# Optimization experiments

Measured on AMD Instinct MI355X. Metric: run time of the kernel, lower is better.

The kernel has to match this reference:

```python
import jax, jax.numpy as jnp
import numpy as np

B, S, DIN, DQ, DK = 8, 2048, 1024, 64, 64

def setup_inputs() -> dict:
    key = jax.random.key(0)
    ks = jax.random.split(key, 8)
    sc = 0.02
    return {
        "input_tensor": jax.random.normal(ks[0], (B, S, DIN), jnp.float32),
        "attention_mask": jax.random.randint(ks[1], (B, 1, S), 0, 2) == 1,
        "Wq": jax.random.normal(ks[2], (DIN, DQ), jnp.float32) * sc,
        "bq": jnp.zeros((DQ,), jnp.float32),
        "Wk": jax.random.normal(ks[3], (DIN, DK), jnp.float32) * sc,
        "bk": jnp.zeros((DK,), jnp.float32),
        "Wv": jax.random.normal(ks[4], (DIN, DK), jnp.float32) * sc,
        "bv": jnp.zeros((DK,), jnp.float32),
    }

def reference(input_tensor, attention_mask, Wq, bq, Wk, bk, Wv, bv):
    q = input_tensor @ Wq + bq          # [B,S,DQ]
    k = input_tensor @ Wk + bk          # [B,S,DK]
    v = input_tensor @ Wv + bv          # [B,S,DK]
    # NOTE: original scales by sqrt(query.size(1)) == sqrt(seq_len), faithfully kept
    scale = q.shape[1] ** 0.5
    scores = jnp.einsum('bqd,bkd->bqk', q, k) / scale
    scores = jnp.where(attention_mask, jnp.float32(-1e9), scores)
    attn = jax.nn.softmax(scores, axis=-1)
    context = jnp.einsum('bqk,bkd->bqd', attn, v)
    return context
```

## Files before the change

### kernel.cpp

```cpp
#include <hip/hip_runtime.h>
#include <hip/hip_bf16.h>

#define NB 8
#define SEQ 2048
#define DIN 1024
#define DH 64

typedef __attribute__((ext_vector_type(8))) short bf16x8;
typedef __attribute__((ext_vector_type(4))) float f32x4;

static __device__ __forceinline__ unsigned short f2bf(float f) {
    unsigned int u = __builtin_bit_cast(unsigned int, f);
    unsigned int r = (u + 0x7FFFu + ((u >> 16) & 1u)) >> 16;
    return (unsigned short)r;
}

static __device__ __forceinline__ unsigned int cvt_pk_bf16(float lo, float hi) {
    unsigned int d;
    asm volatile("v_cvt_pk_bf16_f32 %0, %1, %2" : "=v"(d) : "v"(lo), "v"(hi));
    return d;
}

__global__ __launch_bounds__(256) void prep_kernel(
    const float* __restrict__ Wq, const float* __restrict__ Wk, const float* __restrict__ Wv,
    unsigned short* __restrict__ Wfrag)
{
    int j = blockIdx.x * 256 + threadIdx.x;
    int mat = j >> 16;
    int rem = j & 65535;
    int k = rem >> 6;
    int c = rem & 63;
    const float* W = (mat == 0) ? Wq : ((mat == 1) ? Wk : Wv);
    float v = W[rem];
    int col = mat * 64 + c;
    int cg = col >> 4, cl = col & 15;
    int kk = k >> 5, kq = (k >> 3) & 3, ke = k & 7;
    Wfrag[(size_t)(cg * 32 + kk) * 512 + cl * 32 + kq * 8 + ke] = f2bf(v);
}

__global__ __launch_bounds__(256, 4) void qkv_kernel(
    const float* __restrict__ X, const unsigned short* __restrict__ Wfrag,
    const float* __restrict__ bq, const float* __restrict__ bk, const float* __restrict__ bv,
    unsigned short* __restrict__ Qb, unsigned short* __restrict__ Kb, unsigned short* __restrict__ Vt)
{
    __shared__ __align__(16) short As[16][128];

    const int tid = threadIdx.x;
    const int w   = tid >> 6;
    const int l15 = tid & 15;
    const int lq  = (tid & 63) >> 4;
    const int row0 = blockIdx.x * 16;

    f32x4 acc[3] = {};

    const int srow = tid >> 4;
    const int scol = (tid & 15) * 8;
    const float* xb = X + (size_t)(row0 + srow) * DIN + scol;
    const int swc = scol ^ ((srow & 7) << 3);

    const unsigned short* wfb[3];
    #pragma unroll
    for (int n = 0; n < 3; ++n)
        wfb[n] = Wfrag + (size_t)((w * 3 + n) * 32) * 512 + (l15 * 4 + lq) * 8;

    float4 pa0 = *(const float4*)(xb);
    float4 pa1 = *(const float4*)(xb + 4);
    float4 pb0 = *(const float4*)(xb + 128);
    float4 pb1 = *(const float4*)(xb + 132);

    #pragma unroll
    for (int step = 0; step < 8; ++step) {
        float4 c0 = (step & 1) ? pb0 : pa0;
        float4 c1 = (step & 1) ? pb1 : pa1;
        unsigned int u0 = cvt_pk_bf16(c0.x, c0.y);
        unsigned int u1 = cvt_pk_bf16(c0.z, c0.w);
        unsigned int u2 = cvt_pk_bf16(c1.x, c1.y);
        unsigned int u3 = cvt_pk_bf16(c1.z, c1.w);

        if (step + 2 < 8) {
            const float* xn = xb + (step + 2) * 128;
            if (step & 1) { pb0 = *(const float4*)(xn); pb1 = *(const float4*)(xn + 4); }
            else          { pa0 = *(const float4*)(xn); pa1 = *(const float4*)(xn + 4); }
        }

        __syncthreads();
        uint4 pk; pk.x = u0; pk.y = u1; pk.z = u2; pk.w = u3;
        *(uint4*)&As[srow][swc] = pk;
        __syncthreads();

        #pragma unroll
        for (int kkl = 0; kkl < 4; ++kkl) {
            bf16x8 bfr[3];
            #pragma unroll
            for (int n = 0; n < 3; ++n)
                bfr[n] = *(const bf16x8*)(wfb[n] + (size_t)(step * 4 + kkl) * 512);
            bf16x8 a = *(const bf16x8*)&As[l15][(kkl * 32 + lq * 8) ^ ((l15 & 7) << 3)];
            #pragma unroll
            for (int n = 0; n < 3; ++n)
                acc[n] = __builtin_amdgcn_mfma_f32_16x16x32_bf16(a, bfr[n], acc[n], 0, 0, 0);
        }
    }

    #pragma unroll
    for (int n = 0; n < 3; ++n) {
        int col = w * 48 + n * 16 + l15;
        int mat = col >> 6, c = col & 63;
        float badd = ((mat == 0) ? bq : ((mat == 1) ? bk : bv))[c];
        #pragma unroll
        for (int reg = 0; reg < 4; ++reg) {
            int row = row0 + lq * 4 + reg;
            unsigned short v16 = f2bf(acc[n][reg] + badd);
            if (mat == 0)      Qb[(size_t)row * DH + c] = v16;
            else if (mat == 1) Kb[(size_t)row * DH + c] = v16;
            else {
                int bb = row >> 11, ss = row & 2047;
                Vt[((size_t)(bb * DH + c)) * SEQ + ss] = v16;
            }
        }
    }
}

#define KT 128
#define NT (SEQ / KT)
#define PPITCH 36

__global__ __launch_bounds__(512, 2) void attn_kernel(
    const unsigned short* __restrict__ Qb, const unsigned short* __restrict__ Kb,
    const unsigned short* __restrict__ Vt, const int* __restrict__ mask,
    float* __restrict__ out)
{
    __shared__ __align__(16) unsigned char smem[65536 + 8 * 32 * PPITCH * 2 + 8 * 32 * 4];
    short (*Ks)[KT][DH]     = reinterpret_cast<short (*)[KT][DH]>(smem);
    short (*Vs)[DH][KT]     = reinterpret_cast<short (*)[DH][KT]>(smem + 32768);
    short (*ps)[32][PPITCH] = reinterpret_cast<short (*)[32][PPITCH]>(smem + 65536);
    float (*sml)[32]        = reinterpret_cast<float (*)[32]>(smem + 65536 + 8 * 32 * PPITCH * 2);
    float (*so)[64][64]     = reinterpret_cast<float (*)[64][64]>(smem);

    const int tid = threadIdx.x;
    const int w   = tid >> 6;
    const int l   = tid & 63;
    const int l15 = l & 15;
    const int lq  = l >> 4;
    const int wqh = w >> 2;
    const int wkq = w & 3;

    int bid = blockIdx.x;
    bid = (bid & 7) * 32 + (bid >> 3);
    const int b  = bid >> 5;
    const int q0 = (bid & 31) * 64;

    bf16x8 aq[2][2];
    #pragma unroll
    for (int m = 0; m < 2; ++m)
        #pragma unroll
        for (int kk = 0; kk < 2; ++kk)
            aq[m][kk] = *(const bf16x8*)(Qb + ((size_t)(b * SEQ + q0 + wqh * 32 + m * 16 + l15)) * DH + kk * 32 + lq * 8);

    const int krow = tid >> 3;
    const int kcol = (tid & 7) * 8;
    const int kdst = kcol ^ ((krow & 7) << 3);
    const int vrow = tid >> 4;
    const int vcol = (tid & 15) * 8;
    const int vdst = vcol ^ ((vrow & 7) << 3);

    const unsigned short* Kbase = Kb + (size_t)(b * SEQ) * DH + kcol;
    const unsigned short* Vbase = Vt + (size_t)(b * DH) * SEQ + vcol;

    bf16x8 kr[2], vr[2];
    #pragma unroll
    for (int i = 0; i < 2; ++i) {
        kr[i] = *(const bf16x8*)(Kbase + (size_t)(i * 64 + krow) * DH);
        vr[i] = *(const bf16x8*)(Vbase + (size_t)(i * 32 + vrow) * SEQ);
    }

    f32x4 o[2][4];
    #pragma unroll
    for (int m = 0; m < 2; ++m)
        #pragma unroll
        for (int n = 0; n < 4; ++n) o[m][n] = f32x4{0, 0, 0, 0};
    float lr[2][4] = {};

    const float rscale = 0.022097086912079612f;
    const int kw = wkq * 32;
    const int* mbase = mask + b * SEQ + kw + l15;

    for (int t = 0; t < NT; ++t) {
        const int cur = t & 1;

        #pragma unroll
        for (int i = 0; i < 2; ++i) *(bf16x8*)&Ks[cur][i * 64 + krow][kdst] = kr[i];
        #pragma unroll
        for (int i = 0; i < 2; ++i) *(bf16x8*)&Vs[cur][i * 32 + vrow][vdst] = vr[i];

        int mk0 = mbase[t * KT];
        int mk1 = mbase[t * KT + 16];

        if (t + 1 < NT) {
            const int key0n = (t + 1) * KT;
            #pragma unroll
            for (int i = 0; i < 2; ++i) {
                kr[i] = *(const bf16x8*)(Kbase + (size_t)(key0n + i * 64 + krow) * DH);
                vr[i] = *(const bf16x8*)(Vbase + (size_t)(i * 32 + vrow) * SEQ + key0n);
            }
        }

        __syncthreads();

        bf16x8 bkf[2][2];
        #pragma unroll
        for (int n = 0; n < 2; ++n)
            #pragma unroll
            for (int kk = 0; kk < 2; ++kk)
                bkf[n][kk] = *(const bf16x8*)&Ks[cur][kw + n * 16 + l15][(kk * 32 + lq * 8) ^ ((l15 & 7) << 3)];
        f32x4 s[2][2];
        #pragma unroll
        for (int m = 0; m < 2; ++m)
            #pragma unroll
            for (int n = 0; n < 2; ++n) s[m][n] = f32x4{0, 0, 0, 0};
        #pragma unroll
        for (int kk = 0; kk < 2; ++kk)
            #pragma unroll
            for (int m = 0; m < 2; ++m)
                #pragma unroll
                for (int n = 0; n < 2; ++n)
                    s[m][n] = __builtin_amdgcn_mfma_f32_16x16x32_bf16(aq[m][kk], bkf[n][kk], s[m][n], 0, 0, 0);

        float bb0 = mk0 ? -1e30f : 0.0f;
        float bb1 = mk1 ? -1e30f : 0.0f;
        #pragma unroll
        for (int m = 0; m < 2; ++m)
            #pragma unroll
            for (int n = 0; n < 2; ++n) {
                float bvv = n ? bb1 : bb0;
                #pragma unroll
                for (int r = 0; r < 4; ++r) {
                    float p = __expf(fmaf(s[m][n][r], rscale, bvv));
                    lr[m][r] += p;
                    ps[w][m * 16 + lq * 4 + r][n * 16 + l15] = (short)f2bf(p);
                }
            }

        bf16x8 pa[2];
        #pragma unroll
        for (int m = 0; m < 2; ++m)
            pa[m] = *(const bf16x8*)&ps[w][m * 16 + l15][lq * 8];
        bf16x8 bvf[4];
        #pragma unroll
        for (int n = 0; n < 4; ++n)
            bvf[n] = *(const bf16x8*)&Vs[cur][n * 16 + l15][(kw + lq * 8) ^ ((l15 & 7) << 3)];
        #pragma unroll
        for (int m = 0; m < 2; ++m)
            #pragma unroll
            for (int n = 0; n < 4; ++n)
                o[m][n] = __builtin_amdgcn_mfma_f32_16x16x32_bf16(pa[m], bvf[n], o[m][n], 0, 0, 0);
    }

    #pragma unroll
    for (int off = 1; off < 16; off <<= 1)
        #pragma unroll
        for (int m = 0; m < 2; ++m)
            #pragma unroll
            for (int r = 0; r < 4; ++r) lr[m][r] += __shfl_xor(lr[m][r], off);
    if (l15 == 0) {
        #pragma unroll
        for (int m = 0; m < 2; ++m)
            #pragma unroll
            for (int r = 0; r < 4; ++r) sml[w][m * 16 + lq * 4 + r] = lr[m][r];
    }
    __syncthreads();

    #pragma unroll
    for (int m = 0; m < 2; ++m)
        #pragma unroll
        for (int n = 0; n < 4; ++n)
            #pragma unroll
            for (int r = 0; r < 4; ++r)
                so[wkq][wqh * 32 + m * 16 + lq * 4 + r][n * 16 + l15] = o[m][n][r];
    __syncthreads();

    {
        int q  = tid >> 3;
        int d0 = (tid & 7) * 8;
        int wb = (q >> 5) * 4;
        float lt = sml[wb][q & 31] + sml[wb + 1][q & 31] + sml[wb + 2][q & 31] + sml[wb + 3][q & 31];
        float inv = 1.0f / lt;
        float vx[8];
        #pragma unroll
        for (int j = 0; j < 8; ++j)
            vx[j] = (so[0][q][d0 + j] + so[1][q][d0 + j] + so[2][q][d0 + j] + so[3][q][d0 + j]) * inv;
        float* op = out + ((size_t)(b * SEQ + q0 + q)) * DH + d0;
        float4 r0; r0.x = vx[0]; r0.y = vx[1]; r0.z = vx[2]; r0.w = vx[3];
        float4 r1; r1.x = vx[4]; r1.y = vx[5]; r1.z = vx[6]; r1.w = vx[7];
        *(float4*)op = r0;
        *(float4*)(op + 4) = r1;
    }
}

extern "C" void kernel_launch(void* const* d_in, const int* in_sizes, int n_in,
                              void* d_out, int out_size, void* d_ws, size_t ws_size,
                              hipStream_t stream) {
    const float* X    = (const float*)d_in[0];
    const int*   mask = (const int*)d_in[1];
    const float* Wq   = (const float*)d_in[2];
    const float* bq   = (const float*)d_in[3];
    const float* Wk   = (const float*)d_in[4];
    const float* bk   = (const float*)d_in[5];
    const float* Wv   = (const float*)d_in[6];
    const float* bv   = (const float*)d_in[7];
    float* out = (float*)d_out;

    char* ws = (char*)d_ws;
    unsigned short* Qb = (unsigned short*)(ws);
    unsigned short* Kb = (unsigned short*)(ws + (2u << 20));
    unsigned short* Vt = (unsigned short*)(ws + (4u << 20));
    unsigned short* Wfrag = (unsigned short*)(ws + (6u << 20));

    prep_kernel<<<768, 256, 0, stream>>>(Wq, Wk, Wv, Wfrag);
    qkv_kernel<<<1024, 256, 0, stream>>>(X, Wfrag, bq, bk, bv, Qb, Kb, Vt);
    attn_kernel<<<256, 512, 0, stream>>>(Qb, Kb, Vt, mask, out);
}
```

Measured before the change: 66.98 us.

## Enlarge QKV row tile with weight prefetch; single-buffer attention LDS for occupancy

The QKV projection now handles 32 rows per block instead of 16, with double-buffered LDS for the activation tile and a three-deep register prefetch of weight fragments, so each weight load feeds twice the MFMAs. The attention kernel drops from double-buffered K/V LDS to a single buffer with an extra barrier per tile, and merges partial outputs serially into one padded buffer. Together these halve attention LDS so more blocks can be resident. The cost is more barriers and a serialized reduction in attention, and fewer, heavier QKV blocks.

New measurement: 60.47 us. 9.7% less time.

```diff
diff --git a/kernel.cpp b/kernel.cpp
--- a/kernel.cpp
+++ b/kernel.cpp
@@ -38,66 +38,91 @@
     Wfrag[(size_t)(cg * 32 + kk) * 512 + cl * 32 + kq * 8 + ke] = f2bf(v);
 }
 
-__global__ __launch_bounds__(256, 4) void qkv_kernel(
+__global__ __launch_bounds__(256, 2) void qkv_kernel(
     const float* __restrict__ X, const unsigned short* __restrict__ Wfrag,
     const float* __restrict__ bq, const float* __restrict__ bk, const float* __restrict__ bv,
     unsigned short* __restrict__ Qb, unsigned short* __restrict__ Kb, unsigned short* __restrict__ Vt)
 {
-    __shared__ __align__(16) short As[16][128];
+    __shared__ __align__(16) short As[2][32][128];
 
     const int tid = threadIdx.x;
     const int w   = tid >> 6;
-    const int l15 = tid & 15;
-    const int lq  = (tid & 63) >> 4;
-    const int row0 = blockIdx.x * 16;
-
-    f32x4 acc[3] = {};
-
-    const int srow = tid >> 4;
-    const int scol = (tid & 15) * 8;
-    const float* xb = X + (size_t)(row0 + srow) * DIN + scol;
-    const int swc = scol ^ ((srow & 7) << 3);
+    const int l   = tid & 63;
+    const int l15 = l & 15;
+    const int lq  = l >> 4;
+    const int row0 = blockIdx.x * 32;
+
+    f32x4 acc[2][3] = {};
+
+    const float* xb = X + (size_t)row0 * DIN;
 
     const unsigned short* wfb[3];
     #pragma unroll
     for (int n = 0; n < 3; ++n)
         wfb[n] = Wfrag + (size_t)((w * 3 + n) * 32) * 512 + (l15 * 4 + lq) * 8;
 
-    float4 pa0 = *(const float4*)(xb);
-    float4 pa1 = *(const float4*)(xb + 4);
-    float4 pb0 = *(const float4*)(xb + 128);
-    float4 pb1 = *(const float4*)(xb + 132);
+    float4 pf[2][4];
+    #pragma unroll
+    for (int i = 0; i < 4; ++i) {
+        int c = tid + 256 * i;
+        const float* p = xb + (size_t)(c >> 5) * DIN + (c & 31) * 4;
+        pf[0][i] = *(const float4*)(p);
+        pf[1][i] = *(const float4*)(p + 128);
+    }
+
+    bf16x8 wb[3][3];
+    #pragma unroll
+    for (int n = 0; n < 3; ++n) wb[0][n] = *(const bf16x8*)(wfb[n]);
+    #pragma unroll
+    for (int n = 0; n < 3; ++n) wb[1][n] = *(const bf16x8*)(wfb[n] + 512);
 
     #pragma unroll
     for (int step = 0; step < 8; ++step) {
-        float4 c0 = (step & 1) ? pb0 : pa0;
-        float4 c1 = (step & 1) ? pb1 : pa1;
-        unsigned int u0 = cvt_pk_bf16(c0.x, c0.y);
-        unsigned int u1 = cvt_pk_bf16(c0.z, c0.w);
-        unsigned int u2 = cvt_pk_bf16(c1.x, c1.y);
-        unsigned int u3 = cvt_pk_bf16(c1.z, c1.w);
-
+        const int pi = step & 1;
+
+        unsigned int u[8];
+        #pragma unroll
+        for (int i = 0; i < 4; ++i) {
+            u[2 * i]     = cvt_pk_bf16(pf[pi][i].x, pf[pi][i].y);
+            u[2 * i + 1] = cvt_pk_bf16(pf[pi][i].z, pf[pi][i].w);
+        }
+        #pragma unroll
+        for (int i = 0; i < 4; ++i) {
+            int c = tid + 256 * i;
+            int r = c >> 5;
+            int bo = ((c & 31) * 8) ^ ((r & 7) << 4);
+            uint2 v2; v2.x = u[2 * i]; v2.y = u[2 * i + 1];
+            *(uint2*)((char*)&As[pi][r][0] + bo) = v2;
+        }
         if (step + 2 < 8) {
-            const float* xn = xb + (step + 2) * 128;
-            if (step & 1) { pb0 = *(const float4*)(xn); pb1 = *(const float4*)(xn + 4); }
-            else          { pa0 = *(const float4*)(xn); pa1 = *(const float4*)(xn + 4); }
-        }
-
+            #pragma unroll
+            for (int i = 0; i < 4; ++i) {
+                int c = tid + 256 * i;
+                pf[pi][i] = *(const float4*)(xb + (size_t)(c >> 5) * DIN + (step + 2) * 128 + (c & 31) * 4);
+            }
+        }
         __syncthreads();
-        uint4 pk; pk.x = u0; pk.y = u1; pk.z = u2; pk.w = u3;
-        *(uint4*)&As[srow][swc] = pk;
-        __syncthreads();
 
         #pragma unroll
         for (int kkl = 0; kkl < 4; ++kkl) {
-            bf16x8 bfr[3];
-            #pragma unroll
-            for (int n = 0; n < 3; ++n)
-                bfr[n] = *(const bf16x8*)(wfb[n] + (size_t)(step * 4 + kkl) * 512);
-            bf16x8 a = *(const bf16x8*)&As[l15][(kkl * 32 + lq * 8) ^ ((l15 & 7) << 3)];
-            #pragma unroll
-            for (int n = 0; n < 3; ++n)
-                acc[n] = __builtin_amdgcn_mfma_f32_16x16x32_bf16(a, bfr[n], acc[n], 0, 0, 0);
+            const int c = step * 4 + kkl;
+            if (c + 2 < 32) {
+                #pragma unroll
+                for (int n = 0; n < 3; ++n)
+                    wb[(c + 2) % 3][n] = *(const bf16x8*)(wfb[n] + (size_t)(c + 2) * 512);
+            }
+            bf16x8 a[2];
+            #pragma unroll
+            for (int m = 0; m < 2; ++m) {
+                int r = m * 16 + l15;
+                int bo = ((kkl * 32 + lq * 8) * 2) ^ ((r & 7) << 4);
+                a[m] = *(const bf16x8*)((const char*)&As[pi][r][0] + bo);
+            }
+            #pragma unroll
+            for (int m = 0; m < 2; ++m)
+                #pragma unroll
+                for (int n = 0; n < 3; ++n)
+                    acc[m][n] = __builtin_amdgcn_mfma_f32_16x16x32_bf16(a[m], wb[c % 3][n], acc[m][n], 0, 0, 0);
         }
     }
 
@@ -107,14 +132,17 @@
         int mat = col >> 6, c = col & 63;
         float badd = ((mat == 0) ? bq : ((mat == 1) ? bk : bv))[c];
         #pragma unroll
-        for (int reg = 0; reg < 4; ++reg) {
-            int row = row0 + lq * 4 + reg;
-            unsigned short v16 = f2bf(acc[n][reg] + badd);
-            if (mat == 0)      Qb[(size_t)row * DH + c] = v16;
-            else if (mat == 1) Kb[(size_t)row * DH + c] = v16;
-            else {
-                int bb = row >> 11, ss = row & 2047;
-                Vt[((size_t)(bb * DH + c)) * SEQ + ss] = v16;
+        for (int m = 0; m < 2; ++m) {
+            #pragma unroll
+            for (int reg = 0; reg < 4; ++reg) {
+                int row = row0 + m * 16 + lq * 4 + reg;
+                unsigned short v16 = f2bf(acc[m][n][reg] + badd);
+                if (mat == 0)      Qb[(size_t)row * DH + c] = v16;
+                else if (mat == 1) Kb[(size_t)row * DH + c] = v16;
+                else {
+                    int bb = row >> 11, ss = row & 2047;
+                    Vt[((size_t)(bb * DH + c)) * SEQ + ss] = v16;
+                }
             }
         }
     }
@@ -124,17 +152,17 @@
 #define NT (SEQ / KT)
 #define PPITCH 36
 
-__global__ __launch_bounds__(512, 2) void attn_kernel(
+__global__ __launch_bounds__(512, 4) void attn_kernel(
     const unsigned short* __restrict__ Qb, const unsigned short* __restrict__ Kb,
     const unsigned short* __restrict__ Vt, const int* __restrict__ mask,
     float* __restrict__ out)
 {
-    __shared__ __align__(16) unsigned char smem[65536 + 8 * 32 * PPITCH * 2 + 8 * 32 * 4];
-    short (*Ks)[KT][DH]     = reinterpret_cast<short (*)[KT][DH]>(smem);
-    short (*Vs)[DH][KT]     = reinterpret_cast<short (*)[DH][KT]>(smem + 32768);
-    short (*ps)[32][PPITCH] = reinterpret_cast<short (*)[32][PPITCH]>(smem + 65536);
-    float (*sml)[32]        = reinterpret_cast<float (*)[32]>(smem + 65536 + 8 * 32 * PPITCH * 2);
-    float (*so)[64][64]     = reinterpret_cast<float (*)[64][64]>(smem);
+    __shared__ __align__(16) unsigned char smem[32768 + 8 * 32 * PPITCH * 2 + 8 * 32 * 4];
+    short (*Ks)[DH]         = reinterpret_cast<short (*)[DH]>(smem);
+    short (*Vs)[KT]         = reinterpret_cast<short (*)[KT]>(smem + 16384);
+    short (*ps)[32][PPITCH] = reinterpret_cast<short (*)[32][PPITCH]>(smem + 32768);
+    float (*sml)[32]        = reinterpret_cast<float (*)[32]>(smem + 32768 + 8 * 32 * PPITCH * 2);
+    float (*Om)[68]         = reinterpret_cast<float (*)[68]>(smem);
 
     const int tid = threadIdx.x;
     const int w   = tid >> 6;
@@ -185,12 +213,10 @@
     const int* mbase = mask + b * SEQ + kw + l15;
 
     for (int t = 0; t < NT; ++t) {
-        const int cur = t & 1;
-
-        #pragma unroll
-        for (int i = 0; i < 2; ++i) *(bf16x8*)&Ks[cur][i * 64 + krow][kdst] = kr[i];
-        #pragma unroll
-        for (int i = 0; i < 2; ++i) *(bf16x8*)&Vs[cur][i * 32 + vrow][vdst] = vr[i];
+        #pragma unroll
+        for (int i = 0; i < 2; ++i) *(bf16x8*)&Ks[i * 64 + krow][kdst] = kr[i];
+        #pragma unroll
+        for (int i = 0; i < 2; ++i) *(bf16x8*)&Vs[i * 32 + vrow][vdst] = vr[i];
 
         int mk0 = mbase[t * KT];
         int mk1 = mbase[t * KT + 16];
@@ -211,7 +237,7 @@
         for (int n = 0; n < 2; ++n)
             #pragma unroll
             for (int kk = 0; kk < 2; ++kk)
-                bkf[n][kk] = *(const bf16x8*)&Ks[cur][kw + n * 16 + l15][(kk * 32 + lq * 8) ^ ((l15 & 7) << 3)];
+                bkf[n][kk] = *(const bf16x8*)&Ks[kw + n * 16 + l15][(kk * 32 + lq * 8) ^ ((l15 & 7) << 3)];
         f32x4 s[2][2];
         #pragma unroll
         for (int m = 0; m < 2; ++m)
@@ -247,12 +273,14 @@
         bf16x8 bvf[4];
         #pragma unroll
         for (int n = 0; n < 4; ++n)
-            bvf[n] = *(const bf16x8*)&Vs[cur][n * 16 + l15][(kw + lq * 8) ^ ((l15 & 7) << 3)];
+            bvf[n] = *(const bf16x8*)&Vs[n * 16 + l15][(kw + lq * 8) ^ ((l15 & 7) << 3)];
         #pragma unroll
         for (int m = 0; m < 2; ++m)
             #pragma unroll
             for (int n = 0; n < 4; ++n)
                 o[m][n] = __builtin_amdgcn_mfma_f32_16x16x32_bf16(pa[m], bvf[n], o[m][n], 0, 0, 0);
+
+        __syncthreads();
     }
 
     #pragma unroll
@@ -267,15 +295,24 @@
             #pragma unroll
             for (int r = 0; r < 4; ++r) sml[w][m * 16 + lq * 4 + r] = lr[m][r];
     }
-    __syncthreads();
-
-    #pragma unroll
-    for (int m = 0; m < 2; ++m)
-        #pragma unroll
-        for (int n = 0; n < 4; ++n)
-            #pragma unroll
-            for (int r = 0; r < 4; ++r)
-                so[wkq][wqh * 32 + m * 16 + lq * 4 + r][n * 16 + l15] = o[m][n][r];
+
+    #pragma unroll
+    for (int rnd = 0; rnd < 4; ++rnd) {
+        __syncthreads();
+        if (wkq == rnd) {
+            #pragma unroll
+            for (int m = 0; m < 2; ++m)
+                #pragma unroll
+                for (int n = 0; n < 4; ++n)
+                    #pragma unroll
+                    for (int r = 0; r < 4; ++r) {
+                        int row = wqh * 32 + m * 16 + lq * 4 + r;
+                        int col = n * 16 + l15;
+                        if (rnd == 0) Om[row][col] = o[m][n][r];
+                        else          Om[row][col] += o[m][n][r];
+                    }
+        }
+    }
     __syncthreads();
 
     {
@@ -286,8 +323,7 @@
         float inv = 1.0f / lt;
         float vx[8];
         #pragma unroll
-        for (int j = 0; j < 8; ++j)
-            vx[j] = (so[0][q][d0 + j] + so[1][q][d0 + j] + so[2][q][d0 + j] + so[3][q][d0 + j]) * inv;
+        for (int j = 0; j < 8; ++j) vx[j] = Om[q][d0 + j] * inv;
         float* op = out + ((size_t)(b * SEQ + q0 + q)) * DH + d0;
         float4 r0; r0.x = vx[0]; r0.y = vx[1]; r0.z = vx[2]; r0.w = vx[3];
         float4 r1; r1.x = vx[4]; r1.y = vx[5]; r1.z = vx[6]; r1.w = vx[7];
@@ -316,6 +352,6 @@
     unsigned short* Wfrag = (unsigned short*)(ws + (6u << 20));
 
     prep_kernel<<<768, 256, 0, stream>>>(Wq, Wk, Wv, Wfrag);
-    qkv_kernel<<<1024, 256, 0, stream>>>(X, Wfrag, bq, bk, bv, Qb, Kb, Vt);
+    qkv_kernel<<<512, 256, 0, stream>>>(X, Wfrag, bq, bk, bv, Qb, Kb, Vt);
     attn_kernel<<<256, 512, 0, stream>>>(Qb, Kb, Vt, mask, out);
 }
```
